# Kernel optimization log

Measured on AMD Instinct MI355X. Metric: run time of the kernel, lower is better.

The kernel has to match this reference:

```python
import jax, jax.numpy as jnp
import numpy as np


def setup_inputs() -> dict:
    key = jax.random.key(0)
    k1, k2 = jax.random.split(key)
    B, D, H, W = 16, 256, 32, 32
    K = 2048
    z = jax.random.normal(k1, (B, D, H, W), dtype=jnp.float32)
    # EmbeddingEMA init: uniform(-1/K, 1/K); plain randn scaled works as a stand-in param
    codebook = jax.random.uniform(k2, (K, D), dtype=jnp.float32,
                                  minval=-1.0 / K, maxval=1.0 / K)
    return {"z": z, "codebook": codebook}


def reference(z, codebook):
    # z: (B, D, H, W) -> (B, H, W, D) -> (n, D)   [normalize == 'none' path]
    B, D, H, W = z.shape
    z_flat = jnp.transpose(z, (0, 2, 3, 1)).reshape(-1, D)          # (n, D)
    z_norm = z_flat
    codebook_norm = codebook                                         # (K, D)

    # squared L2 distance: ||z||^2 + ||c||^2 - 2 z c^T   -> (n, K)
    distance = (jnp.sum(z_norm * z_norm, axis=1, keepdims=True)
                + jnp.sum(codebook_norm * codebook_norm, axis=1)
                - 2.0 * jnp.matmul(z_norm, codebook_norm.T))

    vq_indices = jnp.argmin(distance, axis=1)                        # (n,)
    z_q = codebook_norm[vq_indices]                                  # gather (n, D)

    # straight-through estimator (standard VQ forward output)
    z_q_st = z_norm + jax.lax.stop_gradient(z_q - z_norm)
    out = z_q_st.reshape(B, H, W, D).transpose(0, 3, 1, 2)           # (B, D, H, W)
    return out
```

## Files before the change

kernel.cpp:

```cpp
#include <hip/hip_runtime.h>
#include <stdint.h>


#define D_    256
#define K_    2048
#define HW_   1024
#define MT    64
#define NT    256
#define KT    16
#define SPLIT 2
#define KS    (K_ / SPLIT)
#define CST   260
#define ZSZ   (KT * MT)
#define BUFSZ (ZSZ + KT * CST)
#define NPIX  16384

__device__ __forceinline__ void gload16(const float* g, float* l) {
    auto* gp = reinterpret_cast<const __attribute__((address_space(1))) uint32_t*>(
        reinterpret_cast<uintptr_t>(g));
    auto* lp = reinterpret_cast<__attribute__((address_space(3))) uint32_t*>(
        reinterpret_cast<uintptr_t>(l));
    __builtin_amdgcn_global_load_lds(gp, lp, 16, 0, 0);
}

__device__ __forceinline__ float pw8(const float r[8]) {
    float t01 = __fadd_rn(r[0], r[1]);
    float t23 = __fadd_rn(r[2], r[3]);
    float L   = __fadd_rn(t01, t23);
    float t45 = __fadd_rn(r[4], r[5]);
    float t67 = __fadd_rn(r[6], r[7]);
    float R   = __fadd_rn(t45, t67);
    return __fadd_rn(L, R);
}

__global__ __launch_bounds__(256) void prep_k(const float* __restrict__ z,
                                              const float* __restrict__ cb,
                                              float* __restrict__ ct,
                                              float* __restrict__ An,
                                              float* __restrict__ Bn,
                                              unsigned long long* __restrict__ keys,
                                              int* __restrict__ cnt) {
    __shared__ float t[64][65];
    int tid = threadIdx.x;
    int bx  = blockIdx.x;
    if (bx < 128) {
        if (bx == 0) cnt[tid] = 0;
        int k0 = (bx & 31) << 6;
        int d0 = (bx >> 5) << 6;
        #pragma unroll
        for (int it = 0; it < 4; ++it) {
            int u  = (it << 8) + tid;
            int kk = u >> 4;
            int dd = (u & 15) << 2;
            float4 v = *reinterpret_cast<const float4*>(
                cb + (size_t)(k0 + kk) * D_ + d0 + dd);
            t[kk][dd + 0] = v.x; t[kk][dd + 1] = v.y;
            t[kk][dd + 2] = v.z; t[kk][dd + 3] = v.w;
        }
        __syncthreads();
        #pragma unroll
        for (int it = 0; it < 4; ++it) {
            int u  = (it << 8) + tid;
            int dd = u >> 4;
            int kk = (u & 15) << 2;
            float4 o;
            o.x = t[kk + 0][dd]; o.y = t[kk + 1][dd];
            o.z = t[kk + 2][dd]; o.w = t[kk + 3][dd];
            *reinterpret_cast<float4*>(ct + (size_t)(d0 + dd) * K_ + k0 + kk) = o;
        }
    } else if (bx < 136) {
        int row = (bx - 128) * 256 + tid;
        const float4* p = reinterpret_cast<const float4*>(cb + (size_t)row * D_);
        float rA[8], rB[8];
        #pragma unroll
        for (int j = 0; j < 8; ++j) { rA[j] = 0.f; rB[j] = 0.f; }
        #pragma unroll
        for (int q = 0; q < 64; ++q) {
            float4 v = p[q];
            float pv[4] = {__fmul_rn(v.x, v.x), __fmul_rn(v.y, v.y),
                           __fmul_rn(v.z, v.z), __fmul_rn(v.w, v.w)};
            if (q < 32) {
                #pragma unroll
                for (int l = 0; l < 4; ++l)
                    rA[(4 * q + l) & 7] = __fadd_rn(rA[(4 * q + l) & 7], pv[l]);
            } else {
                #pragma unroll
                for (int l = 0; l < 4; ++l)
                    rB[(4 * q + l) & 7] = __fadd_rn(rB[(4 * q + l) & 7], pv[l]);
            }
        }
        Bn[row] = __fadd_rn(pw8(rA), pw8(rB));
    } else {
        int blk = bx - 136;
        int b   = blk >> 2;
        int hw0 = (blk & 3) << 8;
        keys[(size_t)b * HW_ + hw0 + tid] = 0xFFFFFFFFFFFFFFFFull;
        const float* zb = z + (size_t)b * (D_ * HW_) + hw0 + tid;
        float rA[8], rB[8];
        #pragma unroll
        for (int j = 0; j < 8; ++j) { rA[j] = 0.f; rB[j] = 0.f; }
        #pragma unroll 8
        for (int d = 0; d < 128; ++d) {
            float v = zb[(size_t)d * HW_];
            rA[d & 7] = __fadd_rn(rA[d & 7], __fmul_rn(v, v));
        }
        #pragma unroll 8
        for (int d = 128; d < 256; ++d) {
            float v = zb[(size_t)d * HW_];
            rB[d & 7] = __fadd_rn(rB[d & 7], __fmul_rn(v, v));
        }
        An[(size_t)b * HW_ + hw0 + tid] = __fadd_rn(pw8(rA), pw8(rB));
    }
}

__global__ __launch_bounds__(256, 2) void vq_k(const float* __restrict__ z,
                                               const float* __restrict__ ct,
                                               const float* __restrict__ cb,
                                               const float* __restrict__ An,
                                               const float* __restrict__ Bn,
                                               unsigned long long* __restrict__ keys,
                                               int* __restrict__ cnt,
                                               float* __restrict__ out) {
    __shared__ float smem[2 * BUFSZ];
    __shared__ int sflag;
    float* rs = smem;
    int*   ri = (int*)(smem + MT * 33);
    int*   idxs = ri;

    const int tid  = threadIdx.x;
    const int lane = tid & 63;
    const int w    = tid >> 6;
    const int u    = tid & 7;
    const int tm   = (tid >> 3) & 7;
    const int tn   = u | (w << 3);
    const int blk  = blockIdx.x;
    const int p    = blk >> 1;
    const int s    = blk & 1;
    const int b      = p >> 4;
    const int hwbase = (p & 15) << 6;
    const float* zbase = z + (size_t)b * (D_ * HW_) + hwbase;
    const float* ctS   = ct + s * KS;

    const int q1 = (u < 4) ? u : u + 8;
    const int q2 = u + 4;
    const int p1 = (tm < 4) ? tm : tm + 8;
    const int p2 = tm + 4;
    const int co1 = (w << 6) + (q1 << 2);
    const int co2 = (w << 6) + (q2 << 2);
    const int zo1 = p1 << 2;
    const int zo2 = p2 << 2;

    const float* zsrc = zbase + (size_t)((w << 2) + (lane >> 4)) * HW_
                              + ((lane & 15) << 2);
    const float* csrc = ctS + ((size_t)lane << 2);

    float bs[8]; int bi[8];
    #pragma unroll
    for (int i = 0; i < 8; ++i) { bs[i] = 1e30f; bi[i] = 0; }
    float acc[8][8];
    #pragma unroll
    for (int i = 0; i < 8; ++i)
        #pragma unroll
        for (int j = 0; j < 8; ++j) acc[i][j] = 0.f;

    #define STAGE(ph)                                                         \
        do {                                                                  \
            int buf_ = (ph) & 1, kc_ = (ph) & 15, nc_ = (ph) >> 4;            \
            float* zb_ = smem + buf_ * BUFSZ;                                 \
            float* cb_ = zb_ + ZSZ;                                           \
            gload16(zsrc + (size_t)kc_ * (KT * HW_), zb_ + (w << 2) * MT);    \
            _Pragma("unroll")                                                 \
            for (int r = 0; r < 4; ++r) {                                     \
                int row = (w << 2) + r;                                       \
                gload16(csrc + (size_t)((kc_ << 4) + row) * K_ + nc_ * NT,    \
                        cb_ + row * CST);                                     \
            }                                                                 \
        } while (0)

    STAGE(0);

    for (int ph = 0; ph < 64; ++ph) {
        __syncthreads();
        if (ph < 63) STAGE(ph + 1);
        const float* zb_ = smem + (ph & 1) * BUFSZ;
        const float* cb_ = zb_ + ZSZ;
        #pragma unroll
        for (int d = 0; d < KT; ++d) {
            const float* zr = zb_ + d * MT;
            float4 a0 = *reinterpret_cast<const float4*>(zr + zo1);
            float4 a1 = *reinterpret_cast<const float4*>(zr + zo2);
            const float* cr = cb_ + d * CST;
            float4 b0 = *reinterpret_cast<const float4*>(cr + co1);
            float4 b1 = *reinterpret_cast<const float4*>(cr + co2);
            float av[8] = {a0.x, a0.y, a0.z, a0.w, a1.x, a1.y, a1.z, a1.w};
            float bv[8] = {b0.x, b0.y, b0.z, b0.w, b1.x, b1.y, b1.z, b1.w};
            #pragma unroll
            for (int i = 0; i < 8; ++i)
                #pragma unroll
                for (int j = 0; j < 8; ++j)
                    acc[i][j] = fmaf(av[i], bv[j], acc[i][j]);
        }
        if ((ph & 15) == 15) {
            int nc = ph >> 4;
            #pragma unroll
            for (int j = 0; j < 8; ++j) {
                int cc = (j < 4) ? ((q1 << 2) + j) : ((q2 << 2) + j - 4);
                int ng = s * KS + nc * NT + (w << 6) + cc;
                float bn = Bn[ng];
                #pragma unroll
                for (int i = 0; i < 8; ++i) {
                    int m = (i < 4) ? ((p1 << 2) + i) : ((p2 << 2) + i - 4);
                    float an = An[(size_t)b * HW_ + hwbase + m];
                    float sc = __fsub_rn(__fadd_rn(an, bn),
                                         __fmul_rn(2.0f, acc[i][j]));
                    if (sc < bs[i] || (sc == bs[i] && ng < bi[i])) {
                        bs[i] = sc; bi[i] = ng;
                    }
                }
            }
            #pragma unroll
            for (int i = 0; i < 8; ++i)
                #pragma unroll
                for (int j = 0; j < 8; ++j) acc[i][j] = 0.f;
        }
    }
    #undef STAGE

    __syncthreads();
    #pragma unroll
    for (int i = 0; i < 8; ++i) {
        int m = (i < 4) ? ((p1 << 2) + i) : ((p2 << 2) + i - 4);
        rs[m * 33 + tn] = bs[i];
        ri[m * 33 + tn] = bi[i];
    }
    __syncthreads();
    unsigned long long* keyp = keys + (size_t)b * HW_ + hwbase;
    if (tid < MT) {
        float best = rs[tid * 33];
        int   bidx = ri[tid * 33];
        for (int t = 1; t < 32; ++t) {
            float sv = rs[tid * 33 + t];
            int   ix = ri[tid * 33 + t];
            if (sv < best || (sv == best && ix < bidx)) { best = sv; bidx = ix; }
        }
        unsigned long long key =
            ((unsigned long long)__float_as_uint(best) << 32) | (unsigned)bidx;
        atomicMin(keyp + tid, key);
    }
    __threadfence();
    __syncthreads();
    if (tid == 0) sflag = atomicAdd(cnt + p, 1);
    __syncthreads();
    if (sflag == SPLIT - 1) {
        if (tid < MT) {
            unsigned long long v = atomicMin(keyp + tid, 0xFFFFFFFFFFFFFFFFull);
            idxs[tid] = (int)(unsigned)v;
        }
        __syncthreads();
        float* obase = out + (size_t)b * (D_ * HW_) + hwbase;
        #pragma unroll
        for (int it = 0; it < 16; ++it) {
            int uu = (it << 8) + tid;
            int dd = uu >> 4;
            int c4 = uu & 15;
            int i0 = idxs[(c4 << 2) + 0];
            int i1 = idxs[(c4 << 2) + 1];
            int i2 = idxs[(c4 << 2) + 2];
            int i3 = idxs[(c4 << 2) + 3];
            float4 o;
            o.x = cb[(size_t)i0 * D_ + dd];
            o.y = cb[(size_t)i1 * D_ + dd];
            o.z = cb[(size_t)i2 * D_ + dd];
            o.w = cb[(size_t)i3 * D_ + dd];
            *reinterpret_cast<float4*>(obase + (size_t)dd * HW_ + (c4 << 2)) = o;
        }
    }
}

extern "C" void kernel_launch(void* const* d_in, const int* in_sizes, int n_in,
                              void* d_out, int out_size, void* d_ws, size_t ws_size,
                              hipStream_t stream) {
    const float* z  = (const float*)d_in[0];
    const float* cb = (const float*)d_in[1];
    unsigned long long* keys = (unsigned long long*)d_ws;
    int*   cnt = (int*)(keys + NPIX);
    float* An  = (float*)(cnt + 256);
    float* Bn  = An + NPIX;
    float* ct  = Bn + K_;
    float* out = (float*)d_out;

    prep_k<<<dim3(200), dim3(256), 0, stream>>>(z, cb, ct, An, Bn, keys, cnt);
    vq_k<<<dim3(256 * SPLIT), dim3(256), 0, stream>>>(z, ct, cb, An, Bn,
                                                      keys, cnt, out);
}
```

Baseline: 343.1 us.

## Replace LDS-staged tiles with direct global loads and shuffle-based argmin reduction

The vq kernel no longer stages z and codebook tiles in shared memory with async global-to-LDS loads and double buffering. Each thread now reads its 8x8 operand fragments straight from global memory over the full D loop. The codebook split goes from 2 to 4 blocks per pixel tile, and per-pixel minima are packed into 64-bit keys and reduced with wave shuffles plus a small LDS table. This removes the per-phase barriers and the LDS footprint, but it relies on L1/L2 to absorb heavily redundant global reads, since each z and codebook value is read by many threads.

Measured after the change: 425.1 us. +23.9%, slower.

```diff
diff --git a/kernel.cpp b/kernel.cpp
--- a/kernel.cpp
+++ b/kernel.cpp
@@ -6,22 +6,9 @@
 #define K_    2048
 #define HW_   1024
 #define MT    64
-#define NT    256
-#define KT    16
-#define SPLIT 2
+#define SPLIT 4
 #define KS    (K_ / SPLIT)
-#define CST   260
-#define ZSZ   (KT * MT)
-#define BUFSZ (ZSZ + KT * CST)
 #define NPIX  16384
-
-__device__ __forceinline__ void gload16(const float* g, float* l) {
-    auto* gp = reinterpret_cast<const __attribute__((address_space(1))) uint32_t*>(
-        reinterpret_cast<uintptr_t>(g));
-    auto* lp = reinterpret_cast<__attribute__((address_space(3))) uint32_t*>(
-        reinterpret_cast<uintptr_t>(l));
-    __builtin_amdgcn_global_load_lds(gp, lp, 16, 0, 0);
-}
 
 __device__ __forceinline__ float pw8(const float r[8]) {
     float t01 = __fadd_rn(r[0], r[1]);
@@ -121,77 +108,41 @@
                                                unsigned long long* __restrict__ keys,
                                                int* __restrict__ cnt,
                                                float* __restrict__ out) {
-    __shared__ float smem[2 * BUFSZ];
+    __shared__ unsigned long long kred[MT * 4];
+    __shared__ int idxs[MT];
     __shared__ int sflag;
-    float* rs = smem;
-    int*   ri = (int*)(smem + MT * 33);
-    int*   idxs = ri;
-
-    const int tid  = threadIdx.x;
-    const int lane = tid & 63;
-    const int w    = tid >> 6;
-    const int u    = tid & 7;
-    const int tm   = (tid >> 3) & 7;
-    const int tn   = u | (w << 3);
-    const int blk  = blockIdx.x;
-    const int p    = blk >> 1;
-    const int s    = blk & 1;
+
+    const int tid = threadIdx.x;
+    const int w   = tid >> 6;
+    const int u   = tid & 7;
+    const int tm  = (tid >> 3) & 7;
+    const int tn  = u | (w << 3);
+    const int p   = blockIdx.x >> 2;
+    const int s   = blockIdx.x & 3;
     const int b      = p >> 4;
     const int hwbase = (p & 15) << 6;
-    const float* zbase = z + (size_t)b * (D_ * HW_) + hwbase;
-    const float* ctS   = ct + s * KS;
-
-    const int q1 = (u < 4) ? u : u + 8;
-    const int q2 = u + 4;
-    const int p1 = (tm < 4) ? tm : tm + 8;
-    const int p2 = tm + 4;
-    const int co1 = (w << 6) + (q1 << 2);
-    const int co2 = (w << 6) + (q2 << 2);
-    const int zo1 = p1 << 2;
-    const int zo2 = p2 << 2;
-
-    const float* zsrc = zbase + (size_t)((w << 2) + (lane >> 4)) * HW_
-                              + ((lane & 15) << 2);
-    const float* csrc = ctS + ((size_t)lane << 2);
-
-    float bs[8]; int bi[8];
+
+    const float* zt = z + (size_t)b * (D_ * HW_) + hwbase + (tm << 3);
+    unsigned long long kmin[8];
     #pragma unroll
-    for (int i = 0; i < 8; ++i) { bs[i] = 1e30f; bi[i] = 0; }
-    float acc[8][8];
-    #pragma unroll
-    for (int i = 0; i < 8; ++i)
-        #pragma unroll
-        for (int j = 0; j < 8; ++j) acc[i][j] = 0.f;
-
-    #define STAGE(ph)                                                         \
-        do {                                                                  \
-            int buf_ = (ph) & 1, kc_ = (ph) & 15, nc_ = (ph) >> 4;            \
-            float* zb_ = smem + buf_ * BUFSZ;                                 \
-            float* cb_ = zb_ + ZSZ;                                           \
-            gload16(zsrc + (size_t)kc_ * (KT * HW_), zb_ + (w << 2) * MT);    \
-            _Pragma("unroll")                                                 \
-            for (int r = 0; r < 4; ++r) {                                     \
-                int row = (w << 2) + r;                                       \
-                gload16(csrc + (size_t)((kc_ << 4) + row) * K_ + nc_ * NT,    \
-                        cb_ + row * CST);                                     \
-            }                                                                 \
-        } while (0)
-
-    STAGE(0);
-
-    for (int ph = 0; ph < 64; ++ph) {
-        __syncthreads();
-        if (ph < 63) STAGE(ph + 1);
-        const float* zb_ = smem + (ph & 1) * BUFSZ;
-        const float* cb_ = zb_ + ZSZ;
-        #pragma unroll
-        for (int d = 0; d < KT; ++d) {
-            const float* zr = zb_ + d * MT;
-            float4 a0 = *reinterpret_cast<const float4*>(zr + zo1);
-            float4 a1 = *reinterpret_cast<const float4*>(zr + zo2);
-            const float* cr = cb_ + d * CST;
-            float4 b0 = *reinterpret_cast<const float4*>(cr + co1);
-            float4 b1 = *reinterpret_cast<const float4*>(cr + co2);
+    for (int i = 0; i < 8; ++i) kmin[i] = 0xFFFFFFFFFFFFFFFFull;
+
+    for (int nc = 0; nc < 2; ++nc) {
+        const float* cs = ct + s * KS + nc * 256 + (tn << 3);
+        float acc[8][8];
+        #pragma unroll
+        for (int i = 0; i < 8; ++i)
+            #pragma unroll
+            for (int j = 0; j < 8; ++j) acc[i][j] = 0.f;
+
+        #pragma unroll 4
+        for (int d = 0; d < D_; ++d) {
+            const float* zp = zt + (size_t)d * HW_;
+            const float* cp = cs + (size_t)d * K_;
+            float4 a0 = *reinterpret_cast<const float4*>(zp);
+            float4 a1 = *reinterpret_cast<const float4*>(zp + 4);
+            float4 b0 = *reinterpret_cast<const float4*>(cp);
+            float4 b1 = *reinterpret_cast<const float4*>(cp + 4);
             float av[8] = {a0.x, a0.y, a0.z, a0.w, a1.x, a1.y, a1.z, a1.w};
             float bv[8] = {b0.x, b0.y, b0.z, b0.w, b1.x, b1.y, b1.z, b1.w};
             #pragma unroll
@@ -200,52 +151,45 @@
                 for (int j = 0; j < 8; ++j)
                     acc[i][j] = fmaf(av[i], bv[j], acc[i][j]);
         }
-        if ((ph & 15) == 15) {
-            int nc = ph >> 4;
+        #pragma unroll
+        for (int j = 0; j < 8; ++j) {
+            int ng = s * KS + nc * 256 + (tn << 3) + j;
+            float bn = Bn[ng];
             #pragma unroll
-            for (int j = 0; j < 8; ++j) {
-                int cc = (j < 4) ? ((q1 << 2) + j) : ((q2 << 2) + j - 4);
-                int ng = s * KS + nc * NT + (w << 6) + cc;
-                float bn = Bn[ng];
-                #pragma unroll
-                for (int i = 0; i < 8; ++i) {
-                    int m = (i < 4) ? ((p1 << 2) + i) : ((p2 << 2) + i - 4);
-                    float an = An[(size_t)b * HW_ + hwbase + m];
-                    float sc = __fsub_rn(__fadd_rn(an, bn),
-                                         __fmul_rn(2.0f, acc[i][j]));
-                    if (sc < bs[i] || (sc == bs[i] && ng < bi[i])) {
-                        bs[i] = sc; bi[i] = ng;
-                    }
-                }
+            for (int i = 0; i < 8; ++i) {
+                float an = An[(size_t)b * HW_ + hwbase + (tm << 3) + i];
+                float sc = __fsub_rn(__fadd_rn(an, bn),
+                                     __fmul_rn(2.0f, acc[i][j]));
+                unsigned long long key =
+                    ((unsigned long long)__float_as_uint(sc) << 32) | (unsigned)ng;
+                if (key < kmin[i]) kmin[i] = key;
             }
-            #pragma unroll
-            for (int i = 0; i < 8; ++i)
-                #pragma unroll
-                for (int j = 0; j < 8; ++j) acc[i][j] = 0.f;
-        }
-    }
-    #undef STAGE
-
-    __syncthreads();
+        }
+    }
+
     #pragma unroll
     for (int i = 0; i < 8; ++i) {
-        int m = (i < 4) ? ((p1 << 2) + i) : ((p2 << 2) + i - 4);
-        rs[m * 33 + tn] = bs[i];
-        ri[m * 33 + tn] = bi[i];
+        unsigned long long k = kmin[i], o;
+        o = __shfl_xor(k, 1, 64); if (o < k) k = o;
+        o = __shfl_xor(k, 2, 64); if (o < k) k = o;
+        o = __shfl_xor(k, 4, 64); if (o < k) k = o;
+        kmin[i] = k;
+    }
+    if (u == 0) {
+        #pragma unroll
+        for (int i = 0; i < 8; ++i)
+            kred[((tm << 3) + i) * 4 + w] = kmin[i];
     }
     __syncthreads();
     unsigned long long* keyp = keys + (size_t)b * HW_ + hwbase;
     if (tid < MT) {
-        float best = rs[tid * 33];
-        int   bidx = ri[tid * 33];
-        for (int t = 1; t < 32; ++t) {
-            float sv = rs[tid * 33 + t];
-            int   ix = ri[tid * 33 + t];
-            if (sv < best || (sv == best && ix < bidx)) { best = sv; bidx = ix; }
-        }
-        unsigned long long key =
-            ((unsigned long long)__float_as_uint(best) << 32) | (unsigned)bidx;
-        atomicMin(keyp + tid, key);
+        unsigned long long k2 = kred[tid * 4];
+        #pragma unroll
+        for (int t = 1; t < 4; ++t) {
+            unsigned long long o = kred[tid * 4 + t];
+            if (o < k2) k2 = o;
+        }
+        atomicMin(keyp + tid, k2);
     }
     __threadfence();
     __syncthreads();
```
